# Performance work log

Measured on AMD Instinct MI355X. Metric: run time of the kernel, lower is better.

The kernel has to match this reference:

```python
import jax, jax.numpy as jnp
import numpy as np

B, T, H = 128, 2048, 512

def setup_inputs() -> dict:
    key = jax.random.key(0)
    ks = jax.random.split(key, 7)
    s = 1.0 / np.sqrt(H)
    return {
        "lstm_output": jax.random.normal(ks[0], (B, T, H), dtype=jnp.float32),
        "Wa_w": jax.random.normal(ks[1], (H, H), dtype=jnp.float32) * s,
        "Wa_b": jax.random.normal(ks[2], (H,), dtype=jnp.float32) * s,
        "Ua_w": jax.random.normal(ks[3], (H, H), dtype=jnp.float32) * s,
        "Ua_b": jax.random.normal(ks[4], (H,), dtype=jnp.float32) * s,
        "Va_w": jax.random.normal(ks[5], (1, H), dtype=jnp.float32) * s,
        "Va_b": jax.random.normal(ks[6], (1,), dtype=jnp.float32) * s,
    }

def reference(lstm_output, Wa_w, Wa_b, Ua_w, Ua_b, Va_w, Va_b):
    # Wa(x) + Ua(x) fused into a single GEMM with summed weights/biases
    # (algebraically identical since both act on the same input).
    Wsum = Wa_w + Ua_w            # [H, H]
    bsum = Wa_b + Ua_b            # [H]
    pre = jnp.einsum('bth,oh->bto', lstm_output, Wsum) + bsum  # [B,T,H]
    score = jnp.einsum('bth,h->bt', jnp.tanh(pre), Va_w[0]) + Va_b[0]  # [B,T]
    attention_weights = jax.nn.softmax(score, axis=1)          # [B,T]
    context = jnp.einsum('bt,bth->bh', attention_weights, lstm_output)  # [B,H]
    return (context, attention_weights)
```

## Files before the change

kernel.cpp:

```cpp
#include <hip/hip_runtime.h>
#include <hip/hip_bf16.h>


#define BB 128
#define TT 2048
#define HH 512

typedef __bf16 bf16_t;
typedef __bf16 bf16x4_t __attribute__((ext_vector_type(4)));
typedef __bf16 bf16x8_t __attribute__((ext_vector_type(8)));
typedef float f32x4_t __attribute__((ext_vector_type(4)));

__device__ __forceinline__ float tanh_fast(float x) {
    float e = __expf(2.0f * x);
    return 1.0f - 2.0f * __builtin_amdgcn_rcpf(e + 1.0f);
}

__global__ void prep_kernel(const float* __restrict__ wa, const float* __restrict__ ua,
                            const float* __restrict__ wab, const float* __restrict__ uab,
                            bf16_t* __restrict__ wsum, float* __restrict__ bsum) {
    int i = blockIdx.x * 256 + threadIdx.x;
    wsum[i] = (bf16_t)(wa[i] + ua[i]);
    if (i < HH) bsum[i] = wab[i] + uab[i];
}

__global__ __launch_bounds__(256) void gemm_score_kernel(
    const float* __restrict__ x, const bf16_t* __restrict__ wsum,
    const float* __restrict__ bsum, const float* __restrict__ va,
    float* __restrict__ score) {
    __shared__ __align__(16) bf16_t As[128][72];
    __shared__ __align__(16) bf16_t Bs[128][72];

    const int tid  = threadIdx.x;
    const int lane = tid & 63;
    const int wave = tid >> 6;
    const int wm   = (wave >> 1) * 64;
    const int wn   = (wave & 1) * 64;
    const int quad = lane >> 4;
    const int lo   = lane & 15;
    const int m0   = blockIdx.x * 128;
    const int n0   = blockIdx.y * 128;

    f32x4_t acc[4][4];
#pragma unroll
    for (int mi = 0; mi < 4; ++mi)
#pragma unroll
        for (int ni = 0; ni < 4; ++ni)
            acc[mi][ni] = (f32x4_t){0.f, 0.f, 0.f, 0.f};

    const int ar = tid >> 4;
    const int ac = (tid & 15) * 4;
    const int br = tid >> 3;
    const int bc = (tid & 7) * 8;

    for (int k0 = 0; k0 < HH; k0 += 64) {
#pragma unroll
        for (int p = 0; p < 8; ++p) {
            int row = p * 16 + ar;
            float4 v = *(const float4*)(x + (size_t)(m0 + row) * HH + k0 + ac);
            bf16x4_t bv;
            bv[0] = (bf16_t)v.x; bv[1] = (bf16_t)v.y;
            bv[2] = (bf16_t)v.z; bv[3] = (bf16_t)v.w;
            *(bf16x4_t*)&As[row][ac] = bv;
        }
#pragma unroll
        for (int p = 0; p < 4; ++p) {
            int row = p * 32 + br;
            *(bf16x8_t*)&Bs[row][bc] =
                *(const bf16x8_t*)(wsum + (size_t)(n0 + row) * HH + k0 + bc);
        }
        __syncthreads();

#pragma unroll
        for (int kk = 0; kk < 64; kk += 32) {
            bf16x8_t a[4], b[4];
#pragma unroll
            for (int mi = 0; mi < 4; ++mi)
                a[mi] = *(const bf16x8_t*)&As[wm + mi * 16 + lo][kk + quad * 8];
#pragma unroll
            for (int ni = 0; ni < 4; ++ni)
                b[ni] = *(const bf16x8_t*)&Bs[wn + ni * 16 + lo][kk + quad * 8];
#pragma unroll
            for (int mi = 0; mi < 4; ++mi)
#pragma unroll
                for (int ni = 0; ni < 4; ++ni)
                    acc[mi][ni] = __builtin_amdgcn_mfma_f32_16x16x32_bf16(
                        a[mi], b[ni], acc[mi][ni], 0, 0, 0);
        }
        __syncthreads();
    }

    float bsr[4], var[4];
#pragma unroll
    for (int ni = 0; ni < 4; ++ni) {
        int o = n0 + wn + ni * 16 + lo;
        bsr[ni] = bsum[o];
        var[ni] = va[o];
    }
#pragma unroll
    for (int mi = 0; mi < 4; ++mi) {
#pragma unroll
        for (int r = 0; r < 4; ++r) {
            float s = 0.f;
#pragma unroll
            for (int ni = 0; ni < 4; ++ni)
                s += var[ni] * tanh_fast(acc[mi][ni][r] + bsr[ni]);
            s += __shfl_xor(s, 1);
            s += __shfl_xor(s, 2);
            s += __shfl_xor(s, 4);
            s += __shfl_xor(s, 8);
            if (lo == 0)
                atomicAdd(&score[m0 + wm + mi * 16 + quad * 4 + r], s);
        }
    }
}

__global__ void softmax_kernel(const float* __restrict__ score, float* __restrict__ wout) {
    const int b = blockIdx.x;
    const int tid = threadIdx.x;
    const int lane = tid & 63;
    const int wave = tid >> 6;
    float s[8];
    float mx = -3.4e38f;
#pragma unroll
    for (int i = 0; i < 8; ++i) {
        s[i] = score[b * TT + i * 256 + tid];
        mx = fmaxf(mx, s[i]);
    }
#pragma unroll
    for (int off = 32; off; off >>= 1) mx = fmaxf(mx, __shfl_xor(mx, off));
    __shared__ float rmx[4], rsum[4];
    if (lane == 0) rmx[wave] = mx;
    __syncthreads();
    mx = fmaxf(fmaxf(rmx[0], rmx[1]), fmaxf(rmx[2], rmx[3]));
    float e[8];
    float sum = 0.f;
#pragma unroll
    for (int i = 0; i < 8; ++i) {
        e[i] = __expf(s[i] - mx);
        sum += e[i];
    }
#pragma unroll
    for (int off = 32; off; off >>= 1) sum += __shfl_xor(sum, off);
    if (lane == 0) rsum[wave] = sum;
    __syncthreads();
    sum = rsum[0] + rsum[1] + rsum[2] + rsum[3];
    float inv = 1.0f / sum;
#pragma unroll
    for (int i = 0; i < 8; ++i)
        wout[b * TT + i * 256 + tid] = e[i] * inv;
}

__global__ void context_partial_kernel(const float* __restrict__ x,
                                       const float* __restrict__ w,
                                       float* __restrict__ part) {
    const int b = blockIdx.x, tc = blockIdx.y, tid = threadIdx.x;
    __shared__ float lw[128];
    if (tid < 128) lw[tid] = w[b * TT + tc * 128 + tid];
    __syncthreads();
    const float* xp = x + ((size_t)b * TT + tc * 128) * HH + tid * 2;
    float ax = 0.f, ay = 0.f;
#pragma unroll 4
    for (int i = 0; i < 128; ++i) {
        float2 v = *(const float2*)(xp + (size_t)i * HH);
        float wv = lw[i];
        ax = fmaf(wv, v.x, ax);
        ay = fmaf(wv, v.y, ay);
    }
    float2 o;
    o.x = ax; o.y = ay;
    *(float2*)&part[((size_t)tc * BB + b) * HH + tid * 2] = o;
}

__global__ void context_reduce_kernel(const float* __restrict__ part, float* __restrict__ out) {
    int idx = blockIdx.x * 256 + threadIdx.x;
    float s = 0.f;
#pragma unroll
    for (int tc = 0; tc < 16; ++tc) s += part[tc * (BB * HH) + idx];
    out[idx] = s;
}

extern "C" void kernel_launch(void* const* d_in, const int* in_sizes, int n_in,
                              void* d_out, int out_size, void* d_ws, size_t ws_size,
                              hipStream_t stream) {
    const float* x   = (const float*)d_in[0];
    const float* wa  = (const float*)d_in[1];
    const float* wab = (const float*)d_in[2];
    const float* ua  = (const float*)d_in[3];
    const float* uab = (const float*)d_in[4];
    const float* vaw = (const float*)d_in[5];

    float* ctx_out = (float*)d_out;
    float* w_out   = (float*)d_out + BB * HH;

    char* ws = (char*)d_ws;
    float*  score = (float*)ws;
    bf16_t* wsum  = (bf16_t*)(ws + (1 << 20));
    float*  bsum  = (float*)(ws + (1 << 20) + HH * HH * 2);
    float*  part  = (float*)(ws + (1 << 20) + HH * HH * 2 + 4096);

    hipMemsetAsync(score, 0, (size_t)BB * TT * sizeof(float), stream);
    prep_kernel<<<HH * HH / 256, 256, 0, stream>>>(wa, ua, wab, uab, wsum, bsum);
    gemm_score_kernel<<<dim3(BB * TT / 128, HH / 128), 256, 0, stream>>>(
        x, wsum, bsum, vaw, score);
    softmax_kernel<<<BB, 256, 0, stream>>>(score, w_out);
    context_partial_kernel<<<dim3(BB, 16), 256, 0, stream>>>(x, w_out, part);
    context_reduce_kernel<<<BB * HH / 256, 256, 0, stream>>>(part, ctx_out);
}
```

Before: 1.073 ms.

## Load GEMM operands directly from global into registers, drop LDS staging

The GEMM+score kernel no longer stages tiles through shared memory. Each lane loads its MFMA fragments straight from global memory (fp32 x converted to bf16 in registers, bf16 weights), which removes the barriers and LDS traffic. The grid is transposed so the four N-tiles sharing the same x rows run adjacently, which should help L2 reuse of x. The context partial kernel now uses 128 threads with float4 loads. The cost is uncoalesced, redundant global loads: each x row is re-read by both N-waves and across blocks, with no software prefetch.

```diff
diff --git a/kernel.cpp b/kernel.cpp
--- a/kernel.cpp
+++ b/kernel.cpp
@@ -7,9 +7,9 @@
 #define HH 512
 
 typedef __bf16 bf16_t;
-typedef __bf16 bf16x4_t __attribute__((ext_vector_type(4)));
 typedef __bf16 bf16x8_t __attribute__((ext_vector_type(8)));
 typedef float f32x4_t __attribute__((ext_vector_type(4)));
+typedef float f32x8_t __attribute__((ext_vector_type(8)));
 
 __device__ __forceinline__ float tanh_fast(float x) {
     float e = __expf(2.0f * x);
@@ -28,9 +28,6 @@
     const float* __restrict__ x, const bf16_t* __restrict__ wsum,
     const float* __restrict__ bsum, const float* __restrict__ va,
     float* __restrict__ score) {
-    __shared__ __align__(16) bf16_t As[128][72];
-    __shared__ __align__(16) bf16_t Bs[128][72];
-
     const int tid  = threadIdx.x;
     const int lane = tid & 63;
     const int wave = tid >> 6;
@@ -38,8 +35,8 @@
     const int wn   = (wave & 1) * 64;
     const int quad = lane >> 4;
     const int lo   = lane & 15;
-    const int m0   = blockIdx.x * 128;
-    const int n0   = blockIdx.y * 128;
+    const int n0   = blockIdx.x * 128;
+    const int m0   = blockIdx.y * 128;
 
     f32x4_t acc[4][4];
 #pragma unroll
@@ -48,46 +45,32 @@
         for (int ni = 0; ni < 4; ++ni)
             acc[mi][ni] = (f32x4_t){0.f, 0.f, 0.f, 0.f};
 
-    const int ar = tid >> 4;
-    const int ac = (tid & 15) * 4;
-    const int br = tid >> 3;
-    const int bc = (tid & 7) * 8;
+    const float*  xp[4];
+    const bf16_t* wp[4];
+#pragma unroll
+    for (int mi = 0; mi < 4; ++mi)
+        xp[mi] = x + (size_t)(m0 + wm + mi * 16 + lo) * HH + quad * 8;
+#pragma unroll
+    for (int ni = 0; ni < 4; ++ni)
+        wp[ni] = wsum + (size_t)(n0 + wn + ni * 16 + lo) * HH + quad * 8;
 
-    for (int k0 = 0; k0 < HH; k0 += 64) {
+#pragma unroll 2
+    for (int k = 0; k < HH; k += 32) {
+        bf16x8_t a[4], b[4];
 #pragma unroll
-        for (int p = 0; p < 8; ++p) {
-            int row = p * 16 + ar;
-            float4 v = *(const float4*)(x + (size_t)(m0 + row) * HH + k0 + ac);
-            bf16x4_t bv;
-            bv[0] = (bf16_t)v.x; bv[1] = (bf16_t)v.y;
-            bv[2] = (bf16_t)v.z; bv[3] = (bf16_t)v.w;
-            *(bf16x4_t*)&As[row][ac] = bv;
+        for (int mi = 0; mi < 4; ++mi) {
+            f32x8_t u = *(const f32x8_t*)(xp[mi] + k);
+            a[mi] = __builtin_convertvector(u, bf16x8_t);
         }
 #pragma unroll
-        for (int p = 0; p < 4; ++p) {
-            int row = p * 32 + br;
-            *(bf16x8_t*)&Bs[row][bc] =
-                *(const bf16x8_t*)(wsum + (size_t)(n0 + row) * HH + k0 + bc);
-        }
-        __syncthreads();
-
+        for (int ni = 0; ni < 4; ++ni)
+            b[ni] = *(const bf16x8_t*)(wp[ni] + k);
 #pragma unroll
-        for (int kk = 0; kk < 64; kk += 32) {
-            bf16x8_t a[4], b[4];
-#pragma unroll
-            for (int mi = 0; mi < 4; ++mi)
-                a[mi] = *(const bf16x8_t*)&As[wm + mi * 16 + lo][kk + quad * 8];
+        for (int mi = 0; mi < 4; ++mi)
 #pragma unroll
             for (int ni = 0; ni < 4; ++ni)
-                b[ni] = *(const bf16x8_t*)&Bs[wn + ni * 16 + lo][kk + quad * 8];
-#pragma unroll
-            for (int mi = 0; mi < 4; ++mi)
-#pragma unroll
-                for (int ni = 0; ni < 4; ++ni)
-                    acc[mi][ni] = __builtin_amdgcn_mfma_f32_16x16x32_bf16(
-                        a[mi], b[ni], acc[mi][ni], 0, 0, 0);
-        }
-        __syncthreads();
+                acc[mi][ni] = __builtin_amdgcn_mfma_f32_16x16x32_bf16(
+                    a[mi], b[ni], acc[mi][ni], 0, 0, 0);
     }
 
     float bsr[4], var[4];
@@ -158,18 +141,19 @@
     __shared__ float lw[128];
     if (tid < 128) lw[tid] = w[b * TT + tc * 128 + tid];
     __syncthreads();
-    const float* xp = x + ((size_t)b * TT + tc * 128) * HH + tid * 2;
-    float ax = 0.f, ay = 0.f;
+    const float* xp = x + ((size_t)b * TT + tc * 128) * HH + tid * 4;
+    float a0 = 0.f, a1 = 0.f, a2 = 0.f, a3 = 0.f;
 #pragma unroll 4
     for (int i = 0; i < 128; ++i) {
-        float2 v = *(const float2*)(xp + (size_t)i * HH);
+        f32x4_t v = *(const f32x4_t*)(xp + (size_t)i * HH);
         float wv = lw[i];
-        ax = fmaf(wv, v.x, ax);
-        ay = fmaf(wv, v.y, ay);
+        a0 = fmaf(wv, v[0], a0);
+        a1 = fmaf(wv, v[1], a1);
+        a2 = fmaf(wv, v[2], a2);
+        a3 = fmaf(wv, v[3], a3);
     }
-    float2 o;
-    o.x = ax; o.y = ay;
-    *(float2*)&part[((size_t)tc * BB + b) * HH + tid * 2] = o;
+    f32x4_t o = {a0, a1, a2, a3};
+    *(f32x4_t*)&part[((size_t)tc * BB + b) * HH + tid * 4] = o;
 }
 
 __global__ void context_reduce_kernel(const float* __restrict__ part, float* __restrict__ out) {
@@ -201,9 +185,9 @@
 
     hipMemsetAsync(score, 0, (size_t)BB * TT * sizeof(float), stream);
     prep_kernel<<<HH * HH / 256, 256, 0, stream>>>(wa, ua, wab, uab, wsum, bsum);
-    gemm_score_kernel<<<dim3(BB * TT / 128, HH / 128), 256, 0, stream>>>(
+    gemm_score_kernel<<<dim3(HH / 128, BB * TT / 128), 256, 0, stream>>>(
         x, wsum, bsum, vaw, score);
     softmax_kernel<<<BB, 256, 0, stream>>>(score, w_out);
-    context_partial_kernel<<<dim3(BB, 16), 256, 0, stream>>>(x, w_out, part);
+    context_partial_kernel<<<dim3(BB, 16), 128, 0, stream>>>(x, w_out, part);
     context_reduce_kernel<<<BB * HH / 256, 256, 0, stream>>>(part, ctx_out);
 }
```

After: 1.372 ms. 1.28x slower.
